# Optimization experiments

Hardware: AMD Instinct MI355X
Metric: run time of the kernel (lower is better)

## Reference

```python
import jax, jax.numpy as jnp
import numpy as np

B, S, E, H = 4, 2048, 1024, 16
DK = E // H  # 64


def setup_inputs() -> dict:
    key = jax.random.key(0)
    ks = jax.random.split(key, 6)
    scale = 1.0 / np.sqrt(E)
    return {
        "x": jax.random.normal(ks[0], (B, S, E), dtype=jnp.float32),
        "Wq": jax.random.normal(ks[1], (E, E), dtype=jnp.float32) * scale,
        "Wk": jax.random.normal(ks[2], (E, E), dtype=jnp.float32) * scale,
        "Wv": jax.random.normal(ks[3], (E, E), dtype=jnp.float32) * scale,
        "Wo": jax.random.normal(ks[4], (E, E), dtype=jnp.float32) * scale,
        "theta": jax.random.normal(ks[5], (DK,), dtype=jnp.float32),
    }


def _heads(t):
    # [B,S,E] -> [B,H,S,DK]
    b, s, _ = t.shape
    return t.reshape(b, s, H, DK).transpose(0, 2, 1, 3)


def reference(x, Wq, Wk, Wv, Wo, theta):
    # nn.Linear (no bias): y = x @ W.T
    # quantum transform: independent single-qubit RX(x)->RX(theta)->  <Z> = cos(x+theta)
    q = jnp.cos(_heads(x @ Wq.T) + theta)  # [B,H,S,DK]
    k = jnp.cos(_heads(x @ Wk.T) + theta)
    v = jnp.cos(_heads(x @ Wv.T) + theta)
    scores = jnp.einsum("bhqd,bhkd->bhqk", q, k) / jnp.sqrt(jnp.float32(DK))
    attn = jax.nn.softmax(scores, axis=-1)  # dropout is identity in eval
    out = jnp.einsum("bhqk,bhkd->bhqd", attn, v)  # [B,H,S,DK]
    out = out.transpose(0, 2, 1, 3).reshape(x.shape[0], -1, E)
    return out @ Wo.T
```

## Files before the change

### kernel.cpp

```cpp
#include <hip/hip_runtime.h>

#define B_  4
#define S_  2048
#define E_  1024
#define H_  16
#define DK_ 64
#define M_  (B_*S_)

typedef __attribute__((ext_vector_type(8)))  short short8;
typedef __attribute__((ext_vector_type(4)))  float f32x4;
typedef __attribute__((ext_vector_type(16))) float f32x16;

#define QSCALE 0.18033688f

__device__ __forceinline__ unsigned short f2b(float f) {
    union { float f; unsigned u; } v; v.f = f;
    unsigned u = v.u;
    return (unsigned short)((u + 0x7fffu + ((u >> 16) & 1u)) >> 16);
}

__device__ __forceinline__ void gload_lds16(const unsigned short* g, unsigned short* l) {
    __builtin_amdgcn_global_load_lds((const __attribute__((address_space(1))) void*)g,
                                     (__attribute__((address_space(3))) void*)l, 16, 0, 0);
}

#define XN4 (M_*E_/4)
#define WN4 (E_*E_/4)
__global__ __launch_bounds__(256) void cvt_all(
    const float* __restrict__ x,
    const float* __restrict__ w0, const float* __restrict__ w1,
    const float* __restrict__ w2, const float* __restrict__ w3,
    unsigned short* __restrict__ xb, unsigned short* __restrict__ wb,
    unsigned short* __restrict__ wob) {
    int i = blockIdx.x * 256 + threadIdx.x;
    const float* src;
    unsigned short* dst;
    int idx;
    if (i < XN4) { src = x; dst = xb; idx = i; }
    else {
        int j = i - XN4;
        int z = j >> 18;
        idx = j & (WN4 - 1);
        src = (z == 0) ? w0 : (z == 1) ? w1 : (z == 2) ? w2 : w3;
        dst = (z < 3) ? wb + (size_t)z * E_ * E_ : wob;
    }
    float4 f = ((const float4*)src)[idx];
    ushort4 o;
    o.x = f2b(f.x); o.y = f2b(f.y); o.z = f2b(f.z); o.w = f2b(f.w);
    ((ushort4*)dst)[idx] = o;
}

union GemmShm {
    struct { unsigned short As0[8192], Bs0[8192], As1[8192], Bs1[8192]; } kl;
    unsigned short epi[18432];
};

__device__ __forceinline__ void gemm_stage(
    const unsigned short* Ag, const unsigned short* Bg,
    unsigned short* As, unsigned short* Bs, int w, int srow, int sch) {
    #pragma unroll
    for (int c = 0; c < 4; c++) {
        int ro = (w*32 + c*8 + srow);
        gload_lds16(Ag + (size_t)ro*E_ + sch, As + (w*32 + c*8)*64);
        gload_lds16(Bg + (size_t)ro*E_ + sch, Bs + (w*32 + c*8)*64);
    }
}

__device__ __forceinline__ void gemm_compute(
    const unsigned short* As, const unsigned short* Bs,
    f32x4 (&acc)[4][4], int wm, int wn, int col, int quad, int rsw) {
    #pragma unroll
    for (int kk = 0; kk < 64; kk += 32) {
        short8 a[4], b[4];
        #pragma unroll
        for (int i = 0; i < 4; i++)
            a[i] = *(const short8*)&As[(wm + i*16 + col)*64 + ((((kk>>3) + quad) ^ rsw) * 8)];
        #pragma unroll
        for (int j = 0; j < 4; j++)
            b[j] = *(const short8*)&Bs[(wn + j*16 + col)*64 + ((((kk>>3) + quad) ^ rsw) * 8)];
        __builtin_amdgcn_s_setprio(1);
        #pragma unroll
        for (int i = 0; i < 4; i++)
            #pragma unroll
            for (int j = 0; j < 4; j++)
                acc[i][j] = __builtin_amdgcn_mfma_f32_16x16x32_bf16(a[i], b[j], acc[i][j], 0, 0, 0);
        __builtin_amdgcn_s_setprio(0);
    }
}

__global__ __launch_bounds__(256) void gemm_qkv(
    const unsigned short* __restrict__ xb,
    const unsigned short* __restrict__ Wb,
    const float* __restrict__ theta,
    unsigned short* __restrict__ qb,
    unsigned short* __restrict__ kb,
    unsigned short* __restrict__ vtb)
{
    __shared__ GemmShm shm;
    const int tid = threadIdx.x;
    const int w = tid >> 6, lane = tid & 63, quad = lane >> 4, col = lane & 15;
    const int wm = (w & 1) * 64, wn = (w >> 1) * 64;
    const int m0 = blockIdx.x * 128, n0 = blockIdx.y * 128, z = blockIdx.z;
    const unsigned short* Wz = Wb + (size_t)z * E_ * E_;
    const int srow = lane >> 3;
    const int sch  = ((lane & 7) ^ srow) * 8;
    const int rsw  = col & 7;

    const unsigned short* Ag = xb + (size_t)m0 * E_;
    const unsigned short* Bg = Wz + (size_t)n0 * E_;

    f32x4 acc[4][4] = {};
    gemm_stage(Ag, Bg, shm.kl.As0, shm.kl.Bs0, w, srow, sch);
    __syncthreads();
    for (int k0 = 0; k0 < E_; k0 += 128) {
        gemm_stage(Ag + k0 + 64, Bg + k0 + 64, shm.kl.As1, shm.kl.Bs1, w, srow, sch);
        gemm_compute(shm.kl.As0, shm.kl.Bs0, acc, wm, wn, col, quad, rsw);
        __syncthreads();
        if (k0 + 128 < E_)
            gemm_stage(Ag + k0 + 128, Bg + k0 + 128, shm.kl.As0, shm.kl.Bs0, w, srow, sch);
        gemm_compute(shm.kl.As1, shm.kl.Bs1, acc, wm, wn, col, quad, rsw);
        __syncthreads();
    }

    unsigned short* ep = shm.epi;
    const int bblk = m0 >> 11;
    const int sbase = m0 & (S_-1);

    if (z != 2) {
        const float qs = (z == 0) ? QSCALE : 1.0f;
        #pragma unroll
        for (int j = 0; j < 4; j++) {
            int nl = wn + j*16 + col;
            float th = theta[(n0 + nl) & 63];
            #pragma unroll
            for (int i = 0; i < 4; i++)
                #pragma unroll
                for (int r = 0; r < 4; r++) {
                    int ml = wm + i*16 + quad*4 + r;
                    int nls = nl ^ (((ml >> 2) & 3) << 4);
                    ep[ml*144 + nls] = f2b(__cosf(acc[i][j][r] + th) * qs);
                }
        }
        __syncthreads();
        unsigned short* dst = (z == 0) ? qb : kb;
        const int h0 = n0 >> 6;
        #pragma unroll
        for (int k = 0; k < 8; k++) {
            int idx = k*256 + tid;
            int chunk = idx & 7, seg = idx >> 3;
            int ml = seg >> 1, hh = seg & 1;
            int ch = chunk ^ (((ml >> 2) & 3) << 1);
            int4 val = *(const int4*)&ep[ml*144 + hh*64 + ch*8];
            size_t g = ((size_t)(bblk*H_ + h0 + hh)*S_ + sbase + ml)*DK_ + chunk*8;
            *(int4*)&dst[g] = val;
        }
    } else {
        #pragma unroll
        for (int j = 0; j < 4; j++) {
            int nl = wn + j*16 + col;
            float th = theta[(n0 + nl) & 63];
            #pragma unroll
            for (int i = 0; i < 4; i++)
                #pragma unroll
                for (int r = 0; r < 4; r++)
                    ep[nl*136 + wm + i*16 + quad*4 + r] = f2b(__cosf(acc[i][j][r] + th));
        }
        __syncthreads();
        int row = tid >> 1, halfm = (tid & 1) * 64;
        int n = n0 + row, h = n >> 6, d = n & 63;
        size_t base = ((size_t)(bblk*H_ + h)*DK_ + d)*S_ + sbase + halfm;
        #pragma unroll
        for (int k = 0; k < 8; k++)
            *(int4*)&vtb[base + k*8] = *(const int4*)&ep[row*136 + halfm + k*8];
    }
}

__global__ __launch_bounds__(256) void gemm_out(
    const unsigned short* __restrict__ ctx,
    const unsigned short* __restrict__ Wob,
    float* __restrict__ out)
{
    __shared__ GemmShm shm;
    const int tid = threadIdx.x;
    const int w = tid >> 6, lane = tid & 63, quad = lane >> 4, col = lane & 15;
    const int wm = (w & 1) * 64, wn = (w >> 1) * 64;
    const int m0 = blockIdx.x * 128, n0 = blockIdx.y * 128;
    const int srow = lane >> 3;
    const int sch  = ((lane & 7) ^ srow) * 8;
    const int rsw  = col & 7;

    const unsigned short* Ag = ctx + (size_t)m0 * E_;
    const unsigned short* Bg = Wob + (size_t)n0 * E_;

    f32x4 acc[4][4] = {};
    gemm_stage(Ag, Bg, shm.kl.As0, shm.kl.Bs0, w, srow, sch);
    __syncthreads();
    for (int k0 = 0; k0 < E_; k0 += 128) {
        gemm_stage(Ag + k0 + 64, Bg + k0 + 64, shm.kl.As1, shm.kl.Bs1, w, srow, sch);
        gemm_compute(shm.kl.As0, shm.kl.Bs0, acc, wm, wn, col, quad, rsw);
        __syncthreads();
        if (k0 + 128 < E_)
            gemm_stage(Ag + k0 + 128, Bg + k0 + 128, shm.kl.As0, shm.kl.Bs0, w, srow, sch);
        gemm_compute(shm.kl.As1, shm.kl.Bs1, acc, wm, wn, col, quad, rsw);
        __syncthreads();
    }
    #pragma unroll
    for (int j = 0; j < 4; j++) {
        int n = n0 + wn + j*16 + col;
        #pragma unroll
        for (int i = 0; i < 4; i++)
            #pragma unroll
            for (int r = 0; r < 4; r++) {
                int m = m0 + wm + i*16 + quad*4 + r;
                out[(size_t)m*E_ + n] = acc[i][j][r];
            }
    }
}

#define LPK 72
#define LPV 136
#define KVB 128

__global__ __launch_bounds__(256, 2) void flash_attn(
    const unsigned short* __restrict__ qb,
    const unsigned short* __restrict__ kb,
    const unsigned short* __restrict__ vtb,
    unsigned short* __restrict__ ctx)
{
    __shared__ unsigned short Kt[2][KVB*LPK];
    __shared__ unsigned short Vt[2][64*LPV];
    const int tid = threadIdx.x;
    const int w = tid >> 6, lane = tid & 63, col = lane & 31, half = lane >> 5;

    const int f   = blockIdx.y * gridDim.x + blockIdx.x;
    const int swz = (f & 7) * 64 + (f >> 3);
    const int q0  = (swz & 7) * 256;
    const int bh  = swz >> 3;

    const unsigned short* kbase = kb  + (size_t)bh * S_ * DK_;
    const unsigned short* vbase = vtb + (size_t)bh * DK_ * S_;

    short8 qf[2][4];
    {
        const unsigned short* qrow = qb + ((size_t)bh*S_ + q0 + w*64 + col)*DK_;
        #pragma unroll
        for (int s = 0; s < 2; s++)
            #pragma unroll
            for (int c = 0; c < 4; c++)
                qf[s][c] = *(const short8*)&qrow[(size_t)s*32*DK_ + c*16 + half*8];
    }

    union U8 { unsigned u[4]; short8 s8; };
    U8 ones;
    #pragma unroll
    for (int i = 0; i < 4; i++) ones.u[i] = 0x3F803F80u;

    f32x16 oacc[2][2] = {};
    f32x16 lacc[2] = {};

    #pragma unroll
    for (int j = 0; j < 4; j++) {
        int s = tid + j*256;
        int krow = s >> 3, kc8 = (s & 7) * 8;
        int vrow = s >> 4, vc8 = (s & 15) * 8;
        *(int4*)&Kt[0][krow*LPK + kc8] = *(const int4*)&kbase[(size_t)krow*DK_ + kc8];
        *(int4*)&Vt[0][vrow*LPV + vc8] = *(const int4*)&vbase[(size_t)vrow*S_ + vc8];
    }
    __syncthreads();

    for (int it = 0; it < S_/KVB; ++it) {
        const int cur = it & 1, nxt = cur ^ 1;
        const int ktn = it*KVB + KVB;
        int4 rk[4], rv[4];
        if (ktn < S_) {
            #pragma unroll
            for (int j = 0; j < 4; j++) {
                int s = tid + j*256;
                int krow = s >> 3, kc8 = (s & 7) * 8;
                int vrow = s >> 4, vc8 = (s & 15) * 8;
                rk[j] = *(const int4*)&kbase[(size_t)(ktn + krow)*DK_ + kc8];
                rv[j] = *(const int4*)&vbase[(size_t)vrow*S_ + ktn + vc8];
            }
        }

        #pragma unroll
        for (int t = 0; t < 4; t++) {
            f32x16 sa0 = {}, sa1 = {};
            __builtin_amdgcn_s_setprio(1);
            #pragma unroll
            for (int c = 0; c < 4; c++) {
                short8 kf = *(const short8*)&Kt[cur][(t*32 + col)*LPK + c*16 + half*8];
                sa0 = __builtin_amdgcn_mfma_f32_32x32x16_bf16(kf, qf[0][c], sa0, 0, 0, 0);
                sa1 = __builtin_amdgcn_mfma_f32_32x32x16_bf16(kf, qf[1][c], sa1, 0, 0, 0);
            }
            __builtin_amdgcn_s_setprio(0);
            unsigned pk[2][4][2];
            #pragma unroll
            for (int rg = 0; rg < 4; rg++) {
                float a0 = __builtin_amdgcn_exp2f(sa0[rg*4+0]);
                float a1 = __builtin_amdgcn_exp2f(sa0[rg*4+1]);
                float a2 = __builtin_amdgcn_exp2f(sa0[rg*4+2]);
                float a3 = __builtin_amdgcn_exp2f(sa0[rg*4+3]);
                pk[0][rg][0] = __builtin_amdgcn_perm(__float_as_uint(a1), __float_as_uint(a0), 0x07060302u);
                pk[0][rg][1] = __builtin_amdgcn_perm(__float_as_uint(a3), __float_as_uint(a2), 0x07060302u);
                float b0 = __builtin_amdgcn_exp2f(sa1[rg*4+0]);
                float b1 = __builtin_amdgcn_exp2f(sa1[rg*4+1]);
                float b2 = __builtin_amdgcn_exp2f(sa1[rg*4+2]);
                float b3 = __builtin_amdgcn_exp2f(sa1[rg*4+3]);
                pk[1][rg][0] = __builtin_amdgcn_perm(__float_as_uint(b1), __float_as_uint(b0), 0x07060302u);
                pk[1][rg][1] = __builtin_amdgcn_perm(__float_as_uint(b3), __float_as_uint(b2), 0x07060302u);
            }
            #pragma unroll
            for (int kc = 0; kc < 2; kc++) {
                const int lo = 2*kc, hi = 2*kc + 1;
                U8 pa[2];
                #pragma unroll
                for (int s = 0; s < 2; s++) {
                    auto s0 = __builtin_amdgcn_permlane32_swap((int)pk[s][lo][0], (int)pk[s][hi][0], false, false);
                    auto s1 = __builtin_amdgcn_permlane32_swap((int)pk[s][lo][1], (int)pk[s][hi][1], false, false);
                    pa[s].u[0] = (unsigned)s0[0];
                    pa[s].u[1] = (unsigned)s1[0];
                    pa[s].u[2] = (unsigned)s0[1];
                    pa[s].u[3] = (unsigned)s1[1];
                }
                __builtin_amdgcn_s_setprio(1);
                lacc[0] = __builtin_amdgcn_mfma_f32_32x32x16_bf16(pa[0].s8, ones.s8, lacc[0], 0, 0, 0);
                lacc[1] = __builtin_amdgcn_mfma_f32_32x32x16_bf16(pa[1].s8, ones.s8, lacc[1], 0, 0, 0);
                #pragma unroll
                for (int dt = 0; dt < 2; dt++) {
                    short8 vf = *(const short8*)&Vt[cur][(dt*32 + col)*LPV + t*32 + kc*16 + half*8];
                    oacc[0][dt] = __builtin_amdgcn_mfma_f32_32x32x16_bf16(pa[0].s8, vf, oacc[0][dt], 0, 0, 0);
                    oacc[1][dt] = __builtin_amdgcn_mfma_f32_32x32x16_bf16(pa[1].s8, vf, oacc[1][dt], 0, 0, 0);
                }
                __builtin_amdgcn_s_setprio(0);
            }
        }

        if (ktn < S_) {
            #pragma unroll
            for (int j = 0; j < 4; j++) {
                int s = tid + j*256;
                int krow = s >> 3, kc8 = (s & 7) * 8;
                int vrow = s >> 4, vc8 = (s & 15) * 8;
                *(int4*)&Kt[nxt][krow*LPK + kc8] = rk[j];
                *(int4*)&Vt[nxt][vrow*LPV + vc8] = rv[j];
            }
        }
        __syncthreads();
    }

    const int b = bh >> 4, h = bh & 15;
    #pragma unroll
    for (int s = 0; s < 2; s++)
        #pragma unroll
        for (int rg = 0; rg < 4; rg++)
            #pragma unroll
            for (int rr = 0; rr < 4; rr++) {
                int row = rr + rg*8 + half*4;
                float inv = 1.0f / lacc[s][rg*4 + rr];
                int sq = q0 + w*64 + s*32 + row;
                size_t rowoff = ((size_t)(b*S_ + sq))*E_ + h*64;
                #pragma unroll
                for (int dt = 0; dt < 2; dt++)
                    ctx[rowoff + dt*32 + col] = f2b(oacc[s][dt][rg*4 + rr] * inv);
            }
}

extern "C" void kernel_launch(void* const* d_in, const int* in_sizes, int n_in,
                              void* d_out, int out_size, void* d_ws, size_t ws_size,
                              hipStream_t stream) {
    (void)in_sizes; (void)n_in; (void)out_size; (void)ws_size;
    const float* x     = (const float*)d_in[0];
    const float* Wq    = (const float*)d_in[1];
    const float* Wk    = (const float*)d_in[2];
    const float* Wv    = (const float*)d_in[3];
    const float* Wo    = (const float*)d_in[4];
    const float* theta = (const float*)d_in[5];
    float* out = (float*)d_out;

    unsigned short* ws  = (unsigned short*)d_ws;
    unsigned short* xb  = ws;
    unsigned short* Wb  = xb  + (size_t)M_*E_;
    unsigned short* Wob = Wb  + (size_t)3*E_*E_;
    unsigned short* qb  = Wob + (size_t)E_*E_;
    unsigned short* kb  = qb  + (size_t)B_*H_*S_*DK_;
    unsigned short* vtb = kb  + (size_t)B_*H_*S_*DK_;
    unsigned short* ctx = xb;

    cvt_all<<<(XN4 + 4*WN4)/256, 256, 0, stream>>>(x, Wq, Wk, Wv, Wo, xb, Wb, Wob);

    gemm_qkv<<<dim3(M_/128, E_/128, 3), 256, 0, stream>>>(xb, Wb, theta, qb, kb, vtb);
    flash_attn<<<dim3(S_/256, B_*H_), 256, 0, stream>>>(qb, kb, vtb, ctx);
    gemm_out<<<dim3(M_/128, E_/128), 256, 0, stream>>>(ctx, Wob, out);
}
```

Baseline: 247.2 us.

## Use 256x128 GEMM tiles with 8 waves, phased loads and XCD-aware block mapping

Both projection GEMMs move from 128x128 tiles with 4 waves to 256x128 tiles with 8 waves and 512 threads. The K-loop is split into phases that interleave fragment reads, asynchronous global-to-LDS loads and MFMA groups, separated by explicit barriers. Block indices are remapped so neighbouring M tiles land on the same XCD, aiming for better L2 reuse of the shared operands. This raises LDS use and the number of barriers per iteration, and the epilogue indexing is changed to match the larger tile.

```diff
diff --git a/kernel.cpp b/kernel.cpp
--- a/kernel.cpp
+++ b/kernel.cpp
@@ -50,45 +50,119 @@
     ((ushort4*)dst)[idx] = o;
 }
 
-union GemmShm {
-    struct { unsigned short As0[8192], Bs0[8192], As1[8192], Bs1[8192]; } kl;
-    unsigned short epi[18432];
+#define NT 16
+
+struct ShmKL { unsigned short A[2][256*64]; unsigned short B[2][128*64]; };
+union GemmShm8 {
+    ShmKL kl;
+    unsigned short ep[49152];
 };
 
-__device__ __forceinline__ void gemm_stage(
-    const unsigned short* Ag, const unsigned short* Bg,
-    unsigned short* As, unsigned short* Bs, int w, int srow, int sch) {
+__device__ __forceinline__ short8 frag_rd(const unsigned short* S, int row, int kx,
+                                          int quad, int rsw) {
+    return *(const short8*)&S[row*64 + (((kx*4 + quad) ^ rsw) * 8)];
+}
+
+__device__ __forceinline__ void stage8(const unsigned short* Ag, const unsigned short* Bg,
+                                       unsigned short* As, unsigned short* Bs,
+                                       int w, int srow, int sch, int phase) {
+    if (phase == 0) {
+        gload_lds16(Ag + (size_t)(w*32 + 0*8 + srow)*E_ + sch, As + (w*32 + 0*8)*64);
+        gload_lds16(Ag + (size_t)(w*32 + 1*8 + srow)*E_ + sch, As + (w*32 + 1*8)*64);
+    } else if (phase == 1) {
+        gload_lds16(Ag + (size_t)(w*32 + 2*8 + srow)*E_ + sch, As + (w*32 + 2*8)*64);
+        gload_lds16(Ag + (size_t)(w*32 + 3*8 + srow)*E_ + sch, As + (w*32 + 3*8)*64);
+    } else {
+        gload_lds16(Bg + (size_t)(w*16 + 0*8 + srow)*E_ + sch, Bs + (w*16 + 0*8)*64);
+        gload_lds16(Bg + (size_t)(w*16 + 1*8 + srow)*E_ + sch, Bs + (w*16 + 1*8)*64);
+    }
+}
+
+__device__ __forceinline__ void phase_sync() {
+    __builtin_amdgcn_s_barrier();
+    asm volatile("s_waitcnt lgkmcnt(0)" ::: "memory");
+    __builtin_amdgcn_sched_barrier(0);
+}
+
+__device__ __forceinline__ void quad_mfma(f32x4 (&acc)[4][4], const short8 (&a)[4][2],
+                                          const short8 (&b)[4][2], int IH, int JH) {
+    __builtin_amdgcn_s_setprio(1);
     #pragma unroll
-    for (int c = 0; c < 4; c++) {
-        int ro = (w*32 + c*8 + srow);
-        gload_lds16(Ag + (size_t)ro*E_ + sch, As + (w*32 + c*8)*64);
-        gload_lds16(Bg + (size_t)ro*E_ + sch, Bs + (w*32 + c*8)*64);
-    }
-}
-
-__device__ __forceinline__ void gemm_compute(
-    const unsigned short* As, const unsigned short* Bs,
-    f32x4 (&acc)[4][4], int wm, int wn, int col, int quad, int rsw) {
-    #pragma unroll
-    for (int kk = 0; kk < 64; kk += 32) {
-        short8 a[4], b[4];
-        #pragma unroll
-        for (int i = 0; i < 4; i++)
-            a[i] = *(const short8*)&As[(wm + i*16 + col)*64 + ((((kk>>3) + quad) ^ rsw) * 8)];
-        #pragma unroll
-        for (int j = 0; j < 4; j++)
-            b[j] = *(const short8*)&Bs[(wn + j*16 + col)*64 + ((((kk>>3) + quad) ^ rsw) * 8)];
-        __builtin_amdgcn_s_setprio(1);
-        #pragma unroll
-        for (int i = 0; i < 4; i++)
-            #pragma unroll
-            for (int j = 0; j < 4; j++)
-                acc[i][j] = __builtin_amdgcn_mfma_f32_16x16x32_bf16(a[i], b[j], acc[i][j], 0, 0, 0);
-        __builtin_amdgcn_s_setprio(0);
-    }
-}
-
-__global__ __launch_bounds__(256) void gemm_qkv(
+    for (int kx = 0; kx < 2; kx++)
+        #pragma unroll
+        for (int ii = 0; ii < 2; ii++)
+            #pragma unroll
+            for (int jj = 0; jj < 2; jj++)
+                acc[IH*2+ii][JH*2+jj] = __builtin_amdgcn_mfma_f32_16x16x32_bf16(
+                    a[IH*2+ii][kx], b[JH*2+jj][kx], acc[IH*2+ii][JH*2+jj], 0, 0, 0);
+    __builtin_amdgcn_s_setprio(0);
+}
+
+__device__ __forceinline__ void kloop8(const unsigned short* Ag, const unsigned short* Bg,
+                                       GemmShm8& shm, f32x4 (&acc)[4][4], int w, int lane) {
+    const int quad = lane >> 4, col = lane & 15;
+    const int srow = lane >> 3;
+    const int sch  = ((lane & 7) ^ srow) * 8;
+    const int rsw  = col & 7;
+    const int wm = (w >> 1) * 64;
+    const int wn = (w & 1) * 64;
+
+    stage8(Ag, Bg, shm.kl.A[0], shm.kl.B[0], w, srow, sch, 0);
+    stage8(Ag, Bg, shm.kl.A[0], shm.kl.B[0], w, srow, sch, 1);
+    stage8(Ag, Bg, shm.kl.A[0], shm.kl.B[0], w, srow, sch, 2);
+    asm volatile("s_waitcnt vmcnt(0)" ::: "memory");
+    __builtin_amdgcn_s_barrier();
+
+    for (int t = 0; t < NT; ++t) {
+        const int cur = t & 1;
+        const unsigned short* As = shm.kl.A[cur];
+        const unsigned short* Bs = shm.kl.B[cur];
+        unsigned short* An = shm.kl.A[cur ^ 1];
+        unsigned short* Bn = shm.kl.B[cur ^ 1];
+        const unsigned short* Agn = Ag + t*64 + 64;
+        const unsigned short* Bgn = Bg + t*64 + 64;
+        const bool more = (t + 1 < NT);
+        short8 a[4][2], b[4][2];
+
+        #pragma unroll
+        for (int kx = 0; kx < 2; kx++) {
+            a[0][kx] = frag_rd(As, wm + 0*16 + col, kx, quad, rsw);
+            a[1][kx] = frag_rd(As, wm + 1*16 + col, kx, quad, rsw);
+            b[0][kx] = frag_rd(Bs, wn + 0*16 + col, kx, quad, rsw);
+            b[1][kx] = frag_rd(Bs, wn + 1*16 + col, kx, quad, rsw);
+        }
+        if (more) stage8(Agn, Bgn, An, Bn, w, srow, sch, 0);
+        phase_sync();
+        quad_mfma(acc, a, b, 0, 0);
+        __builtin_amdgcn_s_barrier();
+
+        #pragma unroll
+        for (int kx = 0; kx < 2; kx++) {
+            b[2][kx] = frag_rd(Bs, wn + 2*16 + col, kx, quad, rsw);
+            b[3][kx] = frag_rd(Bs, wn + 3*16 + col, kx, quad, rsw);
+        }
+        if (more) stage8(Agn, Bgn, An, Bn, w, srow, sch, 1);
+        phase_sync();
+        quad_mfma(acc, a, b, 0, 1);
+        __builtin_amdgcn_s_barrier();
+
+        #pragma unroll
+        for (int kx = 0; kx < 2; kx++) {
+            a[2][kx] = frag_rd(As, wm + 2*16 + col, kx, quad, rsw);
+            a[3][kx] = frag_rd(As, wm + 3*16 + col, kx, quad, rsw);
+        }
+        if (more) stage8(Agn, Bgn, An, Bn, w, srow, sch, 2);
+        phase_sync();
+        quad_mfma(acc, a, b, 1, 0);
+        __builtin_amdgcn_s_barrier();
+
+        quad_mfma(acc, a, b, 1, 1);
+        asm volatile("s_waitcnt vmcnt(0)" ::: "memory");
+        __builtin_amdgcn_s_barrier();
+    }
+}
+
+__global__ __launch_bounds__(512, 2) void gemm_qkv(
     const unsigned short* __restrict__ xb,
     const unsigned short* __restrict__ Wb,
     const float* __restrict__ theta,
@@ -96,33 +170,25 @@
     unsigned short* __restrict__ kb,
     unsigned short* __restrict__ vtb)
 {
-    __shared__ GemmShm shm;
+    __shared__ GemmShm8 shm;
     const int tid = threadIdx.x;
     const int w = tid >> 6, lane = tid & 63, quad = lane >> 4, col = lane & 15;
-    const int wm = (w & 1) * 64, wn = (w >> 1) * 64;
-    const int m0 = blockIdx.x * 128, n0 = blockIdx.y * 128, z = blockIdx.z;
-    const unsigned short* Wz = Wb + (size_t)z * E_ * E_;
-    const int srow = lane >> 3;
-    const int sch  = ((lane & 7) ^ srow) * 8;
-    const int rsw  = col & 7;
+    const int wm = (w >> 1) * 64, wn = (w & 1) * 64;
+
+    const int f = blockIdx.x;
+    const int xcd = f & 7, idx = f >> 3;
+    const int m0 = (xcd*4 + (idx & 3)) * 256;
+    const int nz = idx >> 2;
+    const int n0 = (nz & 7) * 128;
+    const int z  = nz >> 3;
 
     const unsigned short* Ag = xb + (size_t)m0 * E_;
-    const unsigned short* Bg = Wz + (size_t)n0 * E_;
+    const unsigned short* Bg = Wb + (size_t)z * E_ * E_ + (size_t)n0 * E_;
 
     f32x4 acc[4][4] = {};
-    gemm_stage(Ag, Bg, shm.kl.As0, shm.kl.Bs0, w, srow, sch);
-    __syncthreads();
-    for (int k0 = 0; k0 < E_; k0 += 128) {
-        gemm_stage(Ag + k0 + 64, Bg + k0 + 64, shm.kl.As1, shm.kl.Bs1, w, srow, sch);
-        gemm_compute(shm.kl.As0, shm.kl.Bs0, acc, wm, wn, col, quad, rsw);
-        __syncthreads();
-        if (k0 + 128 < E_)
-            gemm_stage(Ag + k0 + 128, Bg + k0 + 128, shm.kl.As0, shm.kl.Bs0, w, srow, sch);
-        gemm_compute(shm.kl.As1, shm.kl.Bs1, acc, wm, wn, col, quad, rsw);
-        __syncthreads();
-    }
-
-    unsigned short* ep = shm.epi;
+    kloop8(Ag, Bg, shm, acc, w, lane);
+
+    unsigned short* ep = shm.ep;
     const int bblk = m0 >> 11;
     const int sbase = m0 & (S_-1);
 
@@ -146,8 +212,8 @@
         const int h0 = n0 >> 6;
         #pragma unroll
         for (int k = 0; k < 8; k++) {
-            int idx = k*256 + tid;
-            int chunk = idx & 7, seg = idx >> 3;
+            int idx2 = k*512 + tid;
+            int chunk = idx2 & 7, seg = idx2 >> 3;
             int ml = seg >> 1, hh = seg & 1;
             int ch = chunk ^ (((ml >> 2) & 3) << 1);
             int4 val = *(const int4*)&ep[ml*144 + hh*64 + ch*8];
@@ -163,47 +229,39 @@
             for (int i = 0; i < 4; i++)
                 #pragma unroll
                 for (int r = 0; r < 4; r++)
-                    ep[nl*136 + wm + i*16 + quad*4 + r] = f2b(__cosf(acc[i][j][r] + th));
+                    ep[nl*264 + wm + i*16 + quad*4 + r] = f2b(__cosf(acc[i][j][r] + th));
         }
         __syncthreads();
-        int row = tid >> 1, halfm = (tid & 1) * 64;
+        int row = tid >> 2, halfm = (tid & 3) * 64;
         int n = n0 + row, h = n >> 6, d = n & 63;
         size_t base = ((size_t)(bblk*H_ + h)*DK_ + d)*S_ + sbase + halfm;
         #pragma unroll
         for (int k = 0; k < 8; k++)
-            *(int4*)&vtb[base + k*8] = *(const int4*)&ep[row*136 + halfm + k*8];
-    }
-}
-
-__global__ __launch_bounds__(256) void gemm_out(
+            *(int4*)&vtb[base + k*8] = *(const int4*)&ep[row*264 + halfm + k*8];
+    }
+}
+
+__global__ __launch_bounds__(512, 2) void gemm_out(
     const unsigned short* __restrict__ ctx,
     const unsigned short* __restrict__ Wob,
     float* __restrict__ out)
 {
-    __shared__ GemmShm shm;
+    __shared__ GemmShm8 shm;
     const int tid = threadIdx.x;
     const int w = tid >> 6, lane = tid & 63, quad = lane >> 4, col = lane & 15;
-    const int wm = (w & 1) * 64, wn = (w >> 1) * 64;
-    const int m0 = blockIdx.x * 128, n0 = blockIdx.y * 128;
-    const int srow = lane >> 3;
-    const int sch  = ((lane & 7) ^ srow) * 8;
-    const int rsw  = col & 7;
+    const int wm = (w >> 1) * 64, wn = (w & 1) * 64;
+
+    const int f = blockIdx.x;
+    const int xcd = f & 7, idx = f >> 3;
+    const int m0 = (xcd*4 + (idx & 3)) * 256;
+    const int n0 = (idx >> 2) * 128;
 
     const unsigned short* Ag = ctx + (size_t)m0 * E_;
     const unsigned short* Bg = Wob + (size_t)n0 * E_;
 
     f32x4 acc[4][4] = {};
-    gemm_stage(Ag, Bg, shm.kl.As0, shm.kl.Bs0, w, srow, sch);
-    __syncthreads();
-    for (int k0 = 0; k0 < E_; k0 += 128) {
-        gemm_stage(Ag + k0 + 64, Bg + k0 + 64, shm.kl.As1, shm.kl.Bs1, w, srow, sch);
-        gemm_compute(shm.kl.As0, shm.kl.Bs0, acc, wm, wn, col, quad, rsw);
-        __syncthreads();
-        if (k0 + 128 < E_)
-            gemm_stage(Ag + k0 + 128, Bg + k0 + 128, shm.kl.As0, shm.kl.Bs0, w, srow, sch);
-        gemm_compute(shm.kl.As1, shm.kl.Bs1, acc, wm, wn, col, quad, rsw);
-        __syncthreads();
-    }
+    kloop8(Ag, Bg, shm, acc, w, lane);
+
     #pragma unroll
     for (int j = 0; j < 4; j++) {
         int n = n0 + wn + j*16 + col;
@@ -389,7 +447,7 @@
 
     cvt_all<<<(XN4 + 4*WN4)/256, 256, 0, stream>>>(x, Wq, Wk, Wv, Wo, xb, Wb, Wob);
 
-    gemm_qkv<<<dim3(M_/128, E_/128, 3), 256, 0, stream>>>(xb, Wb, theta, qb, kb, vtb);
+    gemm_qkv<<<768, 512, 0, stream>>>(xb, Wb, theta, qb, kb, vtb);
     flash_attn<<<dim3(S_/256, B_*H_), 256, 0, stream>>>(qb, kb, vtb, ctx);
-    gemm_out<<<dim3(M_/128, E_/128), 256, 0, stream>>>(ctx, Wob, out);
-}
+    gemm_out<<<256, 512, 0, stream>>>(ctx, Wob, out);
+}
```

Result: slower. 257.6 us (+4.2%).

## Split flash attention KV tile across two wave groups with LDS reduction

Applied to the files above, without the earlier changes.

Doubles the flash attention block to 512 threads: two groups of four waves each process half of every 128-key tile for the same 256 queries, then combine their partial output and row-sum accumulators through shared memory before the normalised store. Because the kernel uses a fixed, max-free exp, the partials can simply be added. This raises the number of waves per CU and halves per-thread load work. The cost is an extra LDS reduction at the end, and launch_bounds(512,4) may squeeze registers and cause spills.

```diff
diff --git a/kernel.cpp b/kernel.cpp
--- a/kernel.cpp
+++ b/kernel.cpp
@@ -221,7 +221,7 @@
 #define LPV 136
 #define KVB 128
 
-__global__ __launch_bounds__(256, 2) void flash_attn(
+__global__ __launch_bounds__(512, 4) void flash_attn(
     const unsigned short* __restrict__ qb,
     const unsigned short* __restrict__ kb,
     const unsigned short* __restrict__ vtb,
@@ -231,6 +231,7 @@
     __shared__ unsigned short Vt[2][64*LPV];
     const int tid = threadIdx.x;
     const int w = tid >> 6, lane = tid & 63, col = lane & 31, half = lane >> 5;
+    const int qg = w & 3, kh = w >> 2;
 
     const int f   = blockIdx.y * gridDim.x + blockIdx.x;
     const int swz = (f & 7) * 64 + (f >> 3);
@@ -242,7 +243,7 @@
 
     short8 qf[2][4];
     {
-        const unsigned short* qrow = qb + ((size_t)bh*S_ + q0 + w*64 + col)*DK_;
+        const unsigned short* qrow = qb + ((size_t)bh*S_ + q0 + qg*64 + col)*DK_;
         #pragma unroll
         for (int s = 0; s < 2; s++)
             #pragma unroll
@@ -259,8 +260,8 @@
     f32x16 lacc[2] = {};
 
     #pragma unroll
-    for (int j = 0; j < 4; j++) {
-        int s = tid + j*256;
+    for (int j = 0; j < 2; j++) {
+        int s = tid + j*512;
         int krow = s >> 3, kc8 = (s & 7) * 8;
         int vrow = s >> 4, vc8 = (s & 15) * 8;
         *(int4*)&Kt[0][krow*LPK + kc8] = *(const int4*)&kbase[(size_t)krow*DK_ + kc8];
@@ -271,11 +272,11 @@
     for (int it = 0; it < S_/KVB; ++it) {
         const int cur = it & 1, nxt = cur ^ 1;
         const int ktn = it*KVB + KVB;
-        int4 rk[4], rv[4];
+        int4 rk[2], rv[2];
         if (ktn < S_) {
             #pragma unroll
-            for (int j = 0; j < 4; j++) {
-                int s = tid + j*256;
+            for (int j = 0; j < 2; j++) {
+                int s = tid + j*512;
                 int krow = s >> 3, kc8 = (s & 7) * 8;
                 int vrow = s >> 4, vc8 = (s & 15) * 8;
                 rk[j] = *(const int4*)&kbase[(size_t)(ktn + krow)*DK_ + kc8];
@@ -284,7 +285,8 @@
         }
 
         #pragma unroll
-        for (int t = 0; t < 4; t++) {
+        for (int tt = 0; tt < 2; tt++) {
+            const int t = kh*2 + tt;
             f32x16 sa0 = {}, sa1 = {};
             __builtin_amdgcn_s_setprio(1);
             #pragma unroll
@@ -338,8 +340,8 @@
 
         if (ktn < S_) {
             #pragma unroll
-            for (int j = 0; j < 4; j++) {
-                int s = tid + j*256;
+            for (int j = 0; j < 2; j++) {
+                int s = tid + j*512;
                 int krow = s >> 3, kc8 = (s & 7) * 8;
                 int vrow = s >> 4, vc8 = (s & 15) * 8;
                 *(int4*)&Kt[nxt][krow*LPK + kc8] = rk[j];
@@ -349,21 +351,48 @@
         __syncthreads();
     }
 
-    const int b = bh >> 4, h = bh & 15;
-    #pragma unroll
-    for (int s = 0; s < 2; s++)
-        #pragma unroll
-        for (int rg = 0; rg < 4; rg++)
-            #pragma unroll
-            for (int rr = 0; rr < 4; rr++) {
-                int row = rr + rg*8 + half*4;
-                float inv = 1.0f / lacc[s][rg*4 + rr];
-                int sq = q0 + w*64 + s*32 + row;
-                size_t rowoff = ((size_t)(b*S_ + sq))*E_ + h*64;
-                #pragma unroll
-                for (int dt = 0; dt < 2; dt++)
-                    ctx[rowoff + dt*32 + col] = f2b(oacc[s][dt][rg*4 + rr] * inv);
-            }
+    float* fs = (float*)&Kt[0][0];
+    #pragma unroll
+    for (int s = 0; s < 2; s++) {
+        __syncthreads();
+        if (kh == 1) {
+            float* p = fs + ((size_t)qg*64 + lane)*49;
+            #pragma unroll
+            for (int dt = 0; dt < 2; dt++)
+                #pragma unroll
+                for (int r = 0; r < 16; r++) p[dt*16 + r] = oacc[s][dt][r];
+            #pragma unroll
+            for (int r = 0; r < 16; r++) p[32 + r] = lacc[s][r];
+        }
+        __syncthreads();
+        if (kh == 0) {
+            const float* p = fs + ((size_t)qg*64 + lane)*49;
+            #pragma unroll
+            for (int dt = 0; dt < 2; dt++)
+                #pragma unroll
+                for (int r = 0; r < 16; r++) oacc[s][dt][r] += p[dt*16 + r];
+            #pragma unroll
+            for (int r = 0; r < 16; r++) lacc[s][r] += p[32 + r];
+        }
+    }
+
+    if (kh == 0) {
+        const int b = bh >> 4, h = bh & 15;
+        #pragma unroll
+        for (int s = 0; s < 2; s++)
+            #pragma unroll
+            for (int rg = 0; rg < 4; rg++)
+                #pragma unroll
+                for (int rr = 0; rr < 4; rr++) {
+                    int row = rr + rg*8 + half*4;
+                    float inv = 1.0f / lacc[s][rg*4 + rr];
+                    int sq = q0 + qg*64 + s*32 + row;
+                    size_t rowoff = ((size_t)(b*S_ + sq))*E_ + h*64;
+                    #pragma unroll
+                    for (int dt = 0; dt < 2; dt++)
+                        ctx[rowoff + dt*32 + col] = f2b(oacc[s][dt][rg*4 + rr] * inv);
+                }
+    }
 }
 
 extern "C" void kernel_launch(void* const* d_in, const int* in_sizes, int n_in,
@@ -390,6 +419,6 @@
     cvt_all<<<(XN4 + 4*WN4)/256, 256, 0, stream>>>(x, Wq, Wk, Wv, Wo, xb, Wb, Wob);
 
     gemm_qkv<<<dim3(M_/128, E_/128, 3), 256, 0, stream>>>(xb, Wb, theta, qb, kb, vtb);
-    flash_attn<<<dim3(S_/256, B_*H_), 256, 0, stream>>>(qb, kb, vtb, ctx);
+    flash_attn<<<dim3(S_/256, B_*H_), 512, 0, stream>>>(qb, kb, vtb, ctx);
     gemm_out<<<dim3(M_/128, E_/128), 256, 0, stream>>>(ctx, Wob, out);
 }
```

Result: slower. 869.4 us (+251.7%).

## Use 256x128 GEMM tiles with triple-buffered LDS pipeline and XCD-aware block mapping

Applied to the files above, without the earlier changes.

Both projection GEMMs move from 128x128 tiles with 4 waves and double buffering to 256x128 tiles with 8 waves and a three-stage LDS ring. The ring is driven by explicit vmcnt waits and raw s_barrier calls, so only one barrier is needed per K-step. Block indices are remapped so that blocks sharing an A row-panel land on the same XCD, which aims for better L2 reuse. The change uses more LDS per block (about 96KB) and two blocks per CU with 512 threads, and the manual waitcnt scheme could introduce subtle ordering hazards.

```diff
diff --git a/kernel.cpp b/kernel.cpp
--- a/kernel.cpp
+++ b/kernel.cpp
@@ -50,20 +50,22 @@
     ((ushort4*)dst)[idx] = o;
 }
 
-union GemmShm {
-    struct { unsigned short As0[8192], Bs0[8192], As1[8192], Bs1[8192]; } kl;
-    unsigned short epi[18432];
+#define NT 16
+
+union GemmShm3 {
+    struct { unsigned short A[3][256*64]; unsigned short B[3][128*64]; } kl;
+    unsigned short ep[49152];
 };
 
-__device__ __forceinline__ void gemm_stage(
-    const unsigned short* Ag, const unsigned short* Bg,
-    unsigned short* As, unsigned short* Bs, int w, int srow, int sch) {
-    #pragma unroll
-    for (int c = 0; c < 4; c++) {
-        int ro = (w*32 + c*8 + srow);
-        gload_lds16(Ag + (size_t)ro*E_ + sch, As + (w*32 + c*8)*64);
-        gload_lds16(Bg + (size_t)ro*E_ + sch, Bs + (w*32 + c*8)*64);
-    }
+__device__ __forceinline__ void stage6(const unsigned short* Ag, const unsigned short* Bg,
+                                       unsigned short* As, unsigned short* Bs,
+                                       int w, int srow, int sch) {
+    #pragma unroll
+    for (int c = 0; c < 4; c++)
+        gload_lds16(Ag + (size_t)(w*32 + c*8 + srow)*E_ + sch, As + (w*32 + c*8)*64);
+    #pragma unroll
+    for (int c = 0; c < 2; c++)
+        gload_lds16(Bg + (size_t)(w*16 + c*8 + srow)*E_ + sch, Bs + (w*16 + c*8)*64);
 }
 
 __device__ __forceinline__ void gemm_compute(
@@ -88,7 +90,41 @@
     }
 }
 
-__global__ __launch_bounds__(256) void gemm_qkv(
+__device__ __forceinline__ void kloop3(const unsigned short* Ag, const unsigned short* Bg,
+                                       GemmShm3& shm, f32x4 (&acc)[4][4], int w, int lane) {
+    const int quad = lane >> 4, col = lane & 15;
+    const int srow = lane >> 3;
+    const int sch  = ((lane & 7) ^ srow) * 8;
+    const int rsw  = col & 7;
+    const int wm = (w >> 1) * 64, wn = (w & 1) * 64;
+
+    unsigned short *A0 = shm.kl.A[0], *A1 = shm.kl.A[1], *A2 = shm.kl.A[2];
+    unsigned short *B0 = shm.kl.B[0], *B1 = shm.kl.B[1], *B2 = shm.kl.B[2];
+
+    stage6(Ag,      Bg,      A0, B0, w, srow, sch);
+    stage6(Ag + 64, Bg + 64, A1, B1, w, srow, sch);
+    asm volatile("s_waitcnt vmcnt(6)" ::: "memory");
+    __builtin_amdgcn_s_barrier();
+    __builtin_amdgcn_sched_barrier(0);
+
+    for (int t = 0; t < NT; ++t) {
+        if (t + 2 < NT)
+            stage6(Ag + (t+2)*64, Bg + (t+2)*64, A2, B2, w, srow, sch);
+        __builtin_amdgcn_sched_barrier(0);
+
+        gemm_compute(A0, B0, acc, wm, wn, col, quad, rsw);
+
+        if (t + 2 < NT) asm volatile("s_waitcnt vmcnt(6)" ::: "memory");
+        else            asm volatile("s_waitcnt vmcnt(0)" ::: "memory");
+        __builtin_amdgcn_s_barrier();
+        __builtin_amdgcn_sched_barrier(0);
+
+        unsigned short* tA = A0; A0 = A1; A1 = A2; A2 = tA;
+        unsigned short* tB = B0; B0 = B1; B1 = B2; B2 = tB;
+    }
+}
+
+__global__ __launch_bounds__(512, 2) void gemm_qkv(
     const unsigned short* __restrict__ xb,
     const unsigned short* __restrict__ Wb,
     const float* __restrict__ theta,
@@ -96,33 +132,25 @@
     unsigned short* __restrict__ kb,
     unsigned short* __restrict__ vtb)
 {
-    __shared__ GemmShm shm;
+    __shared__ GemmShm3 shm;
     const int tid = threadIdx.x;
     const int w = tid >> 6, lane = tid & 63, quad = lane >> 4, col = lane & 15;
-    const int wm = (w & 1) * 64, wn = (w >> 1) * 64;
-    const int m0 = blockIdx.x * 128, n0 = blockIdx.y * 128, z = blockIdx.z;
-    const unsigned short* Wz = Wb + (size_t)z * E_ * E_;
-    const int srow = lane >> 3;
-    const int sch  = ((lane & 7) ^ srow) * 8;
-    const int rsw  = col & 7;
+    const int wm = (w >> 1) * 64, wn = (w & 1) * 64;
+
+    const int f = blockIdx.x;
+    const int xcd = f & 7, idx = f >> 3;
+    const int m0 = (xcd*4 + (idx & 3)) * 256;
+    const int nz = idx >> 2;
+    const int n0 = (nz & 7) * 128;
+    const int z  = nz >> 3;
 
     const unsigned short* Ag = xb + (size_t)m0 * E_;
-    const unsigned short* Bg = Wz + (size_t)n0 * E_;
+    const unsigned short* Bg = Wb + (size_t)z * E_ * E_ + (size_t)n0 * E_;
 
     f32x4 acc[4][4] = {};
-    gemm_stage(Ag, Bg, shm.kl.As0, shm.kl.Bs0, w, srow, sch);
-    __syncthreads();
-    for (int k0 = 0; k0 < E_; k0 += 128) {
-        gemm_stage(Ag + k0 + 64, Bg + k0 + 64, shm.kl.As1, shm.kl.Bs1, w, srow, sch);
-        gemm_compute(shm.kl.As0, shm.kl.Bs0, acc, wm, wn, col, quad, rsw);
-        __syncthreads();
-        if (k0 + 128 < E_)
-            gemm_stage(Ag + k0 + 128, Bg + k0 + 128, shm.kl.As0, shm.kl.Bs0, w, srow, sch);
-        gemm_compute(shm.kl.As1, shm.kl.Bs1, acc, wm, wn, col, quad, rsw);
-        __syncthreads();
-    }
-
-    unsigned short* ep = shm.epi;
+    kloop3(Ag, Bg, shm, acc, w, lane);
+
+    unsigned short* ep = shm.ep;
     const int bblk = m0 >> 11;
     const int sbase = m0 & (S_-1);
 
@@ -146,8 +174,8 @@
         const int h0 = n0 >> 6;
         #pragma unroll
         for (int k = 0; k < 8; k++) {
-            int idx = k*256 + tid;
-            int chunk = idx & 7, seg = idx >> 3;
+            int idx2 = k*512 + tid;
+            int chunk = idx2 & 7, seg = idx2 >> 3;
             int ml = seg >> 1, hh = seg & 1;
             int ch = chunk ^ (((ml >> 2) & 3) << 1);
             int4 val = *(const int4*)&ep[ml*144 + hh*64 + ch*8];
@@ -163,47 +191,39 @@
             for (int i = 0; i < 4; i++)
                 #pragma unroll
                 for (int r = 0; r < 4; r++)
-                    ep[nl*136 + wm + i*16 + quad*4 + r] = f2b(__cosf(acc[i][j][r] + th));
+                    ep[nl*264 + wm + i*16 + quad*4 + r] = f2b(__cosf(acc[i][j][r] + th));
         }
         __syncthreads();
-        int row = tid >> 1, halfm = (tid & 1) * 64;
+        int row = tid >> 2, halfm = (tid & 3) * 64;
         int n = n0 + row, h = n >> 6, d = n & 63;
         size_t base = ((size_t)(bblk*H_ + h)*DK_ + d)*S_ + sbase + halfm;
         #pragma unroll
         for (int k = 0; k < 8; k++)
-            *(int4*)&vtb[base + k*8] = *(const int4*)&ep[row*136 + halfm + k*8];
-    }
-}
-
-__global__ __launch_bounds__(256) void gemm_out(
+            *(int4*)&vtb[base + k*8] = *(const int4*)&ep[row*264 + halfm + k*8];
+    }
+}
+
+__global__ __launch_bounds__(512, 2) void gemm_out(
     const unsigned short* __restrict__ ctx,
     const unsigned short* __restrict__ Wob,
     float* __restrict__ out)
 {
-    __shared__ GemmShm shm;
+    __shared__ GemmShm3 shm;
     const int tid = threadIdx.x;
     const int w = tid >> 6, lane = tid & 63, quad = lane >> 4, col = lane & 15;
-    const int wm = (w & 1) * 64, wn = (w >> 1) * 64;
-    const int m0 = blockIdx.x * 128, n0 = blockIdx.y * 128;
-    const int srow = lane >> 3;
-    const int sch  = ((lane & 7) ^ srow) * 8;
-    const int rsw  = col & 7;
+    const int wm = (w >> 1) * 64, wn = (w & 1) * 64;
+
+    const int f = blockIdx.x;
+    const int xcd = f & 7, idx = f >> 3;
+    const int m0 = (xcd*4 + (idx & 3)) * 256;
+    const int n0 = (idx >> 2) * 128;
 
     const unsigned short* Ag = ctx + (size_t)m0 * E_;
     const unsigned short* Bg = Wob + (size_t)n0 * E_;
 
     f32x4 acc[4][4] = {};
-    gemm_stage(Ag, Bg, shm.kl.As0, shm.kl.Bs0, w, srow, sch);
-    __syncthreads();
-    for (int k0 = 0; k0 < E_; k0 += 128) {
-        gemm_stage(Ag + k0 + 64, Bg + k0 + 64, shm.kl.As1, shm.kl.Bs1, w, srow, sch);
-        gemm_compute(shm.kl.As0, shm.kl.Bs0, acc, wm, wn, col, quad, rsw);
-        __syncthreads();
-        if (k0 + 128 < E_)
-            gemm_stage(Ag + k0 + 128, Bg + k0 + 128, shm.kl.As0, shm.kl.Bs0, w, srow, sch);
-        gemm_compute(shm.kl.As1, shm.kl.Bs1, acc, wm, wn, col, quad, rsw);
-        __syncthreads();
-    }
+    kloop3(Ag, Bg, shm, acc, w, lane);
+
     #pragma unroll
     for (int j = 0; j < 4; j++) {
         int n = n0 + wn + j*16 + col;
@@ -389,7 +409,7 @@
 
     cvt_all<<<(XN4 + 4*WN4)/256, 256, 0, stream>>>(x, Wq, Wk, Wv, Wo, xb, Wb, Wob);
 
-    gemm_qkv<<<dim3(M_/128, E_/128, 3), 256, 0, stream>>>(xb, Wb, theta, qb, kb, vtb);
+    gemm_qkv<<<768, 512, 0, stream>>>(xb, Wb, theta, qb, kb, vtb);
     flash_attn<<<dim3(S_/256, B_*H_), 256, 0, stream>>>(qb, kb, vtb, ctx);
-    gemm_out<<<dim3(M_/128, E_/128), 256, 0, stream>>>(ctx, Wob, out);
-}
+    gemm_out<<<256, 512, 0, stream>>>(ctx, Wob, out);
+}
```

After: 251.5 us. No clear change (+1.7%).
